# Kernel tuning notes

Measured on AMD Instinct MI355X. Metric: run time of the kernel, lower is better.

The kernel has to match this reference:

```python
import jax, jax.numpy as jnp
import numpy as np

NUM_HEADS = 12
ROPE_THETA = 100.0

def _rotate_half(x):
    x1 = x[..., ::2]
    x2 = x[..., 1::2]
    return jnp.stack((-x2, x1), axis=-1).reshape(x.shape)

def _apply_rope(x, cos, sin):
    return x * cos + _rotate_half(x) * sin

def _rope_cos_sin(h, w, head_dim, theta):
    quarter = head_dim // 4  # head_dim=64 -> 16 freq bands
    inv_freq = 1.0 / theta ** (jnp.arange(quarter, dtype=jnp.float32) / max(quarter, 1))
    y = jnp.repeat(jnp.arange(h, dtype=jnp.float32), w)   # [h*w]
    xc = jnp.tile(jnp.arange(w, dtype=jnp.float32), h)    # [h*w]
    y_freqs = y[:, None] * inv_freq[None, :]               # [N, quarter]
    x_freqs = xc[:, None] * inv_freq[None, :]
    y_ang = jnp.repeat(y_freqs, 2, axis=-1)                # [N, half]
    x_ang = jnp.repeat(x_freqs, 2, axis=-1)
    ang = jnp.concatenate([y_ang, x_ang], axis=-1)         # [N, head_dim]
    return jnp.cos(ang)[None, None], jnp.sin(ang)[None, None]  # [1,1,N,hd]

def setup_inputs() -> dict:
    key = jax.random.key(0)
    ks = jax.random.split(key, 8)
    B, S, D = 8, 1025, 768
    s = 0.02
    return {
        "x": jax.random.normal(ks[0], (B, S, D), jnp.float32),
        "q_w": jax.random.normal(ks[1], (D, D), jnp.float32) * s,
        "q_b": jax.random.normal(ks[2], (D,), jnp.float32) * s,
        "k_w": jax.random.normal(ks[3], (D, D), jnp.float32) * s,
        "v_w": jax.random.normal(ks[4], (D, D), jnp.float32) * s,
        "v_b": jax.random.normal(ks[5], (D,), jnp.float32) * s,
        "o_w": jax.random.normal(ks[6], (D, D), jnp.float32) * s,
        "o_b": jax.random.normal(ks[7], (D,), jnp.float32) * s,
        "h": 32,
        "w": 32,
        "num_prefix_tokens": 1,
    }

def reference(x, q_w, q_b, k_w, v_w, v_b, o_w, o_b, h, w, num_prefix_tokens):
    B, S, D = x.shape
    H = NUM_HEADS
    hd = D // H
    scale = hd ** -0.5
    p = num_prefix_tokens

    def proj(W, b):
        y = jnp.einsum('bsd,ed->bse', x, W)
        if b is not None:
            y = y + b
        return y.reshape(B, S, H, hd).transpose(0, 2, 1, 3)  # [B,H,S,hd]

    q = proj(q_w, q_b)
    k = proj(k_w, None)
    v = proj(v_w, v_b)

    cos, sin = _rope_cos_sin(h, w, hd, ROPE_THETA)
    q = jnp.concatenate([q[:, :, :p], _apply_rope(q[:, :, p:], cos, sin)], axis=2)
    k = jnp.concatenate([k[:, :, :p], _apply_rope(k[:, :, p:], cos, sin)], axis=2)

    attn = jnp.einsum('bhqd,bhkd->bhqk', q * scale, k)
    attn = jax.nn.softmax(attn, axis=-1)
    out = jnp.einsum('bhqk,bhkd->bhqd', attn, v)
    out = out.transpose(0, 2, 1, 3).reshape(B, S, D)
    return jnp.einsum('bsd,ed->bse', out, o_w) + o_b
```

## Files before the change

### kernel.cpp

```cpp
#include <hip/hip_runtime.h>

typedef unsigned short u16;
typedef unsigned int   u32;
typedef __attribute__((ext_vector_type(4))) short s4;
typedef __attribute__((ext_vector_type(8))) short s8;
typedef __attribute__((ext_vector_type(4))) float f4;
typedef __attribute__((ext_vector_type(16))) float f16v;

#define NB   8
#define SEQ  1025
#define DIM  768
#define NH   12
#define HD   64
#define BPAD 1040
#define MPAD 8320
#define MV   8200
#define SQP  1040
#define SKP  1088
#define NG16 68
#define NQKV 2304
#define BHT  96
#define QSCALE 0.1803368801111204f

__device__ __forceinline__ u16 f2bf(float f) {
  u32 u = __builtin_bit_cast(u32, f);
  u += 0x7fffu + ((u >> 16) & 1u);
  return (u16)(u >> 16);
}
__device__ __forceinline__ float bf2f(u16 h) {
  return __builtin_bit_cast(float, ((u32)h) << 16);
}
__device__ __forceinline__ float exp2f_(float x) {
#if __has_builtin(__builtin_amdgcn_exp2f)
  return __builtin_amdgcn_exp2f(x);
#else
  return exp2f(x);
#endif
}
__device__ __forceinline__ u32 cvtpk(float a, float b) {
  u32 r;
  asm("v_cvt_pk_bf16_f32 %0, %1, %2" : "=v"(r) : "v"(a), "v"(b));
  return r;
}

typedef const __attribute__((address_space(1))) void cas1v;
typedef __attribute__((address_space(3))) void as3v;
__device__ __forceinline__ void gload16(const void* g, void* l) {
  __builtin_amdgcn_global_load_lds((cas1v*)g, (as3v*)l, 16, 0, 0);
}

#define MFMA16(a, b, c) __builtin_amdgcn_mfma_f32_16x16x32_bf16(a, b, c, 0, 0, 0)
#define MFMA32(a, b, c) __builtin_amdgcn_mfma_f32_32x32x16_bf16(a, b, c, 0, 0, 0)

__global__ void conv_x(const float* __restrict__ x, u16* __restrict__ xb) {
  int i = blockIdx.x * 256 + threadIdx.x;
  int e = i * 4;
  int row = e / DIM, col = e - row * DIM;
  int b = row / BPAD, s = row - b * BPAD;
  s4 o;
  if (s < SEQ) {
    float4 v = *(const float4*)(x + ((size_t)(b * SEQ + s)) * DIM + col);
    o[0] = (short)f2bf(v.x); o[1] = (short)f2bf(v.y);
    o[2] = (short)f2bf(v.z); o[3] = (short)f2bf(v.w);
  } else {
    o = (s4){0, 0, 0, 0};
  }
  *(s4*)(xb + e) = o;
}

__global__ void conv_w(const float* __restrict__ qw, const float* __restrict__ kw,
                       const float* __restrict__ vw, const float* __restrict__ ow,
                       const float* __restrict__ qb, const float* __restrict__ vb,
                       u16* __restrict__ wqkv, u16* __restrict__ wo, float* __restrict__ biasq,
                       float2* __restrict__ rt) {
  int i = blockIdx.x * 256 + threadIdx.x;
  wqkv[i]           = f2bf(qw[i]);
  wqkv[i + 589824]  = f2bf(kw[i]);
  wqkv[i + 1179648] = f2bf(vw[i]);
  wo[i]             = f2bf(ow[i]);
  if (i < NQKV) biasq[i] = (i < 768) ? qb[i] : (i < 1536 ? 0.f : vb[i - 1536]);
  if (i < SEQ * 32) {
    int s = i >> 5, jj = i & 31;
    float cs = 1.f, sn = 0.f;
    if (s > 0) {
      int tok = s - 1;
      int pos = (jj < 16) ? (tok >> 5) : (tok & 31);
      int f = jj & 15;
      float ang = (float)pos * __expf((float)f * -0.28782313662425572f);
      __sincosf(ang, &sn, &cs);
    }
    rt[i] = make_float2(cs, sn);
  }
}

template <int MODE>
__global__ __launch_bounds__(256) void gemm_bt(const u16* __restrict__ A, const u16* __restrict__ Bm,
                                               float* __restrict__ Cf, const float* __restrict__ bias,
                                               u16* __restrict__ Ql, u16* __restrict__ Kl,
                                               u16* __restrict__ Vp, const float2* __restrict__ rt,
                                               int N, int K, int Mvalid, int nnt) {
  __shared__ u16 smem[16640];
  u16 (*ct)[130] = (u16(*)[130])smem;
  int tid = threadIdx.x;
  int lane = tid & 63, wave = tid >> 6;
  int g = lane >> 4, c16 = lane & 15;
  int nwg = gridDim.x, orig = blockIdx.x;
  int qd = nwg >> 3, rm = nwg & 7, xcd = orig & 7;
  int wgid = (xcd < rm ? xcd * (qd + 1) : rm * (qd + 1) + (xcd - rm) * qd) + (orig >> 3);
  int m0 = (wgid / nnt) * 128, n0 = (wgid % nnt) * 128;
  int wm = wave >> 1, wn = wave & 1;
  f4 acc[4][4] = {};

  int ldrow = wave * 16 + (lane >> 2);
  int ldk = ((lane & 3) ^ ((ldrow >> 1) & 3)) * 8;
  const u16* Asrc = A + (size_t)(m0 + ldrow) * K + ldk;
  const u16* Bsrc = Bm + (size_t)(n0 + ldrow) * K + ldk;

  auto stage = [&](int buf, int k0) {
    u16* aw = smem + buf * 4096 + wave * 512;
    u16* bw = smem + 8192 + buf * 4096 + wave * 512;
    gload16(Asrc + k0, aw);
    gload16(Asrc + 64 * K + k0, aw + 2048);
    gload16(Bsrc + k0, bw);
    gload16(Bsrc + 64 * K + k0, bw + 2048);
  };

  stage(0, 0);
  __syncthreads();
  int nk = K >> 5;
  int kx = (g ^ ((c16 >> 1) & 3)) * 8;
  for (int t = 0; t < nk; t++) {
    int buf = t & 1;
    if (t + 1 < nk) stage(buf ^ 1, (t + 1) << 5);
    s8 af[4], bf[4];
#pragma unroll
    for (int i = 0; i < 4; i++) {
      af[i] = *(const s8*)(smem + buf * 4096 + (wm * 64 + i * 16 + c16) * 32 + kx);
      bf[i] = *(const s8*)(smem + 8192 + buf * 4096 + (wn * 64 + i * 16 + c16) * 32 + kx);
    }
    __builtin_amdgcn_s_setprio(1);
#pragma unroll
    for (int i = 0; i < 4; i++)
#pragma unroll
      for (int j = 0; j < 4; j++)
        acc[i][j] = MFMA16(af[i], bf[j], acc[i][j]);
    __builtin_amdgcn_s_setprio(0);
    __syncthreads();
  }

  if (MODE == 1) {
#pragma unroll
    for (int i = 0; i < 4; i++)
#pragma unroll
      for (int j = 0; j < 4; j++) {
        int n = n0 + wn * 64 + j * 16 + c16;
        float bv = bias[n];
#pragma unroll
        for (int r = 0; r < 4; r++) {
          int m = m0 + wm * 64 + i * 16 + g * 4 + r;
          if (m < Mvalid) Cf[(size_t)m * N + n] = acc[i][j][r] + bv;
        }
      }
  } else {
    int part = (n0 >= 1536) ? 2 : (n0 >= 768 ? 1 : 0);
    float qs = (part == 0) ? QSCALE : 1.0f;
#pragma unroll
    for (int j = 0; j < 4; j++) {
      int col = wn * 64 + j * 16 + c16;
      float bv = bias[n0 + col];
      int jj = (col & 63) >> 1;
      int odd = col & 1;
#pragma unroll
      for (int i = 0; i < 4; i++) {
        int rowb = wm * 64 + i * 16 + g * 4;
#pragma unroll
        for (int r = 0; r < 4; r++) {
          float v = acc[i][j][r] + bv;
          u16 o;
          if (part < 2) {
            float vp = __shfl_xor(v, 1);
            int m = m0 + rowb + r;
            int s = m % BPAD;
            float2 t = rt[(s < SEQ ? s : SEQ - 1) * 32 + jj];
            float rv = odd ? (v * t.x + vp * t.y) : (v * t.x - vp * t.y);
            o = f2bf(rv * qs);
          } else {
            o = f2bf(v);
          }
          ct[rowb + r][col] = o;
        }
      }
    }
    __syncthreads();
    if (part < 2) {
      u16* dstB = (part == 0) ? Ql : Kl;
      int stride = (part == 0) ? SQP : SKP;
#pragma unroll
      for (int p = 0; p < 8; p++) {
        int task = p * 256 + tid;
        int row = task >> 4, cg = (task & 15) * 8;
        int m = m0 + row, b = m / BPAD, s = m - b * BPAD;
        int n = n0 + cg;
        int hq = (n >> 6) - part * NH;
        s8 v = *(const s8*)&ct[row][cg];
        *(s8*)(dstB + ((size_t)((b * NH + hq) * stride + s)) * HD + (n & 63)) = v;
      }
    } else {
#pragma unroll
      for (int p = 0; p < 4; p++) {
        int task = p * 256 + tid;
        int col = task & 127, rg = task >> 7;
        int mb = m0 + rg * 16, b = mb / BPAD, sb = mb - b * BPAD;
        int g16 = sb >> 4;
        int n = n0 + col;
        int hq = (n >> 6) - 2 * NH;
        s8 o0, o1;
#pragma unroll
        for (int k = 0; k < 16; k++) {
          int mp = (k & 3) | (((k >> 3) & 1) << 2) | (((k >> 2) & 1) << 3);
          u16 val = ct[rg * 16 + k][col];
          if (mp < 8) o0[mp] = (short)val; else o1[mp - 8] = (short)val;
        }
        u16* dst = Vp + ((size_t)((b * NH + hq) * NG16 + g16) * HD + (n & 63)) * 16;
        *(s8*)dst = o0;
        *(s8*)(dst + 8) = o1;
      }
    }
  }
}

__global__ __launch_bounds__(256) void attn_k(const u16* __restrict__ Q, const u16* __restrict__ K,
                                              const u16* __restrict__ Vp, u16* __restrict__ Ao) {
  __shared__ u16 lds[2][2][64 * 64];
  int bh = blockIdx.x;
  int tid = threadIdx.x;
  int wave = tid >> 6, lane = tid & 63;
  int q32 = lane & 31, h = lane >> 5;
  int b = bh / NH, hh = bh % NH;
  int qb = blockIdx.y * 128 + wave * 32;
  if (qb > SEQ - 32) qb = SEQ - 32;
  const u16* Qb = Q + (size_t)bh * SQP * HD;
  const u16* Kb = K + (size_t)bh * SKP * HD;
  const u16* Vb = Vp + (size_t)bh * NG16 * 1024;

  s8 qf[4];
#pragma unroll
  for (int t = 0; t < 4; t++)
    qf[t] = *(const s8*)(Qb + (size_t)(qb + q32) * HD + 16 * t + 8 * h);

  f16v o0 = {}, o1 = {};
  float mrun = -3e38f, lrun = 0.f;
  int swz = (q32 & 7) << 4;

  auto stage = [&](int buf, int c) {
#pragma unroll
    for (int i = 0; i < 2; i++) {
      int sb = i * 4096 + tid * 16;
      int row = sb >> 7;
      int ch = (sb >> 4) & 7;
      int so = (ch ^ (row & 7)) * 8;
      u16* kd = &lds[buf][0][i * 2048 + wave * 512];
      u16* vd = &lds[buf][1][i * 2048 + wave * 512];
      gload16(Kb + (size_t)(c * 64 + row) * HD + so, kd);
      gload16(Vb + c * 4096 + i * 2048 + tid * 8, vd);
    }
  };

  stage(0, 0);
  __syncthreads();

  for (int c = 0; c < 17; c++) {
    int buf = c & 1;
    if (c < 16) stage(buf ^ 1, c + 1);
    const char* Ks = (const char*)&lds[buf][0][0];
    const char* Vs = (const char*)&lds[buf][1][0];

    f16v st0 = {}, st1 = {};
    __builtin_amdgcn_s_setprio(1);
#pragma unroll
    for (int t = 0; t < 4; t++) {
      int off = (32 * t + 16 * h) ^ swz;
      s8 a0 = *(const s8*)(Ks + q32 * 128 + off);
      s8 a1 = *(const s8*)(Ks + (32 + q32) * 128 + off);
      st0 = MFMA32(a0, qf[t], st0);
      st1 = MFMA32(a1, qf[t], st1);
    }
    __builtin_amdgcn_s_setprio(0);

    s8 vf0[4], vf1[4];
#pragma unroll
    for (int s = 0; s < 4; s++) {
      vf0[s] = *(const s8*)(Vs + 2048 * s + 32 * q32 + 16 * h);
      vf1[s] = *(const s8*)(Vs + 2048 * s + 1024 + 32 * q32 + 16 * h);
    }

    if (c == 16) {
      st0[0] = h ? -3e38f : st0[0];
#pragma unroll
      for (int r = 1; r < 16; r++) st0[r] = -3e38f;
#pragma unroll
      for (int r = 0; r < 16; r++) st1[r] = -3e38f;
    }

    float mx[8];
#pragma unroll
    for (int r = 0; r < 8; r++)
      mx[r] = fmaxf(fmaxf(st0[r], st0[r + 8]), fmaxf(st1[r], st1[r + 8]));
#pragma unroll
    for (int w = 4; w >= 1; w >>= 1)
#pragma unroll
      for (int r = 0; r < w; r++) mx[r] = fmaxf(mx[r], mx[r + w]);
    float pmax = fmaxf(mx[0], __shfl_xor(mx[0], 32));

    if (!__all(pmax <= mrun + 11.5f)) {
      float mnew = fmaxf(mrun, pmax);
      float cf = exp2f_(mrun - mnew);
      lrun *= cf;
      mrun = mnew;
#pragma unroll
      for (int r = 0; r < 16; r++) {
        float c2 = __shfl(cf, (r & 3) + 8 * (r >> 2) + 4 * h);
        o0[r] *= c2;
        o1[r] *= c2;
      }
    }

    float sm[8];
#pragma unroll
    for (int r = 0; r < 16; r++) {
      st0[r] = exp2f_(st0[r] - mrun);
      st1[r] = exp2f_(st1[r] - mrun);
    }
#pragma unroll
    for (int r = 0; r < 8; r++) sm[r] = (st0[r] + st0[r + 8]) + (st1[r] + st1[r + 8]);
#pragma unroll
    for (int w = 4; w >= 1; w >>= 1)
#pragma unroll
      for (int r = 0; r < w; r++) sm[r] += sm[r + w];
    lrun += sm[0] + __shfl_xor(sm[0], 32);

    __builtin_amdgcn_s_setprio(1);
#pragma unroll
    for (int s = 0; s < 4; s++) {
      union { s8 v; u32 w[4]; } pa;
#pragma unroll
      for (int i = 0; i < 4; i++) {
        float plo = (s < 2) ? st0[8 * (s & 1) + 2 * i]     : st1[8 * (s & 1) + 2 * i];
        float phi = (s < 2) ? st0[8 * (s & 1) + 2 * i + 1] : st1[8 * (s & 1) + 2 * i + 1];
        pa.w[i] = cvtpk(plo, phi);
      }
      o0 = MFMA32(pa.v, vf0[s], o0);
      o1 = MFMA32(pa.v, vf1[s], o1);
    }
    __builtin_amdgcn_s_setprio(0);
    __syncthreads();
  }

  float rl = 1.0f / lrun;
#pragma unroll
  for (int r = 0; r < 16; r++) {
    int cr = (r & 3) + 8 * (r >> 2) + 4 * h;
    float sc = __shfl(rl, cr);
    u16* dst = Ao + (size_t)(b * SEQ + qb + cr) * DIM + hh * HD;
    dst[q32]      = f2bf(o0[r] * sc);
    dst[32 + q32] = f2bf(o1[r] * sc);
  }
}

extern "C" void kernel_launch(void* const* d_in, const int* in_sizes, int n_in,
                              void* d_out, int out_size, void* d_ws, size_t ws_size,
                              hipStream_t stream) {
  const float* x  = (const float*)d_in[0];
  const float* qw = (const float*)d_in[1];
  const float* qb = (const float*)d_in[2];
  const float* kw = (const float*)d_in[3];
  const float* vw = (const float*)d_in[4];
  const float* vb = (const float*)d_in[5];
  const float* ow = (const float*)d_in[6];
  const float* ob = (const float*)d_in[7];
  float* out = (float*)d_out;

  char* ws = (char*)d_ws;
  u16*    xb   = (u16*)(ws);
  u16*    wqkv = (u16*)(ws + 12779520);
  u16*    wo   = (u16*)(ws + 16318464);
  float*  bq   = (float*)(ws + 17498112);
  float2* rt   = (float2*)(ws + 17507328);
  u16*    Ql   = (u16*)(ws + 17769728);
  u16*    Kl   = (u16*)(ws + 30549248);
  u16*    Vp   = (u16*)(ws + 43918592);
  u16*    Ao   = xb;

  conv_x<<<6240, 256, 0, stream>>>(x, xb);
  conv_w<<<2304, 256, 0, stream>>>(qw, kw, vw, ow, qb, vb, wqkv, wo, bq, rt);
  gemm_bt<2><<<1170, 256, 0, stream>>>(xb, wqkv, nullptr, bq, Ql, Kl, Vp, rt, NQKV, DIM, MPAD, 18);
  attn_k<<<dim3(96, 9), 256, 0, stream>>>(Ql, Kl, Vp, Ao);
  gemm_bt<1><<<390, 256, 0, stream>>>(Ao, wo, out, ob, nullptr, nullptr, nullptr, rt, DIM, DIM, MV, 6);
}
```

Measured before the change: 155.6 us.

## Rewrite QKV GEMM with 256x128 tiles, 512 threads and triple-buffered K=64 pipeline

Replaces the templated QKV projection GEMM with a dedicated kernel that uses 256x128 output tiles over 8 waves, K-steps of 64, and a three-stage LDS ring fed by direct global-to-LDS loads. The loads are interleaved between two MFMA half-phases with explicit barriers and waitcnt. Sequence padding grows from 1040 to 1056 so M divides into 256-row tiles, and the workspace offsets and conversion grid are adjusted to match. The aim is more operand reuse per tile and better overlap of memory loads with MFMA work, at the cost of more padded rows, heavy LDS use (144 KB) that limits occupancy, and fragile hand-placed synchronisation.

```diff
diff --git a/kernel.cpp b/kernel.cpp
--- a/kernel.cpp
+++ b/kernel.cpp
@@ -12,10 +12,10 @@
 #define DIM  768
 #define NH   12
 #define HD   64
-#define BPAD 1040
-#define MPAD 8320
+#define BPAD 1056
+#define MPAD 8448
 #define MV   8200
-#define SQP  1040
+#define SQP  1056
 #define SKP  1088
 #define NG16 68
 #define NQKV 2304
@@ -51,6 +51,7 @@
 
 #define MFMA16(a, b, c) __builtin_amdgcn_mfma_f32_16x16x32_bf16(a, b, c, 0, 0, 0)
 #define MFMA32(a, b, c) __builtin_amdgcn_mfma_f32_32x32x16_bf16(a, b, c, 0, 0, 0)
+#define BAR() __builtin_amdgcn_s_barrier()
 
 __global__ void conv_x(const float* __restrict__ x, u16* __restrict__ xb) {
   int i = blockIdx.x * 256 + threadIdx.x;
@@ -93,14 +94,178 @@
   }
 }
 
-template <int MODE>
-__global__ __launch_bounds__(256) void gemm_bt(const u16* __restrict__ A, const u16* __restrict__ Bm,
-                                               float* __restrict__ Cf, const float* __restrict__ bias,
-                                               u16* __restrict__ Ql, u16* __restrict__ Kl,
-                                               u16* __restrict__ Vp, const float2* __restrict__ rt,
-                                               int N, int K, int Mvalid, int nnt) {
-  __shared__ u16 smem[16640];
+__global__ __launch_bounds__(512, 2) void gemm_qkv(const u16* __restrict__ A, const u16* __restrict__ Bm,
+                                                   const float* __restrict__ bias,
+                                                   u16* __restrict__ Ql, u16* __restrict__ Kl,
+                                                   u16* __restrict__ Vp, const float2* __restrict__ rt) {
+  __shared__ u16 smem[73728];
+  const int K = DIM;
+  int tid = threadIdx.x;
+  int lane = tid & 63, wave = tid >> 6;
+  int g = lane >> 4, c16 = lane & 15;
+  int wm = wave >> 1, wn = wave & 1;
+  int nwg = gridDim.x, orig = blockIdx.x;
+  int qd = nwg >> 3, rm = nwg & 7, xcd = orig & 7;
+  int wgid = (xcd < rm ? xcd * (qd + 1) : rm * (qd + 1) + (xcd - rm) * qd) + (orig >> 3);
+  int m0 = (wgid / 18) * 256, n0 = (wgid % 18) * 128;
+
+  f4 acc[4][4] = {};
+
+  int lr = lane >> 3;
+  int lc = ((lane & 7) ^ lr) * 8;
+  const u16* As0 = A  + (size_t)(m0 + wave * 8 + lr) * K + lc;
+  const u16* Bs0 = Bm + (size_t)(n0 + wave * 8 + lr) * K + lc;
+
+  auto stageA3 = [&](int sb, int ko) {
+    u16* base = smem + sb * 24576 + wave * 512;
+    gload16(As0 + ko,           base);
+    gload16(As0 + 64 * K + ko,  base + 4096);
+    gload16(As0 + 128 * K + ko, base + 8192);
+  };
+  auto stageB3 = [&](int sb, int ko) {
+    u16* baseA = smem + sb * 24576 + wave * 512;
+    u16* baseB = smem + sb * 24576 + 16384 + wave * 512;
+    gload16(As0 + 192 * K + ko, baseA + 12288);
+    gload16(Bs0 + ko,           baseB);
+    gload16(Bs0 + 64 * K + ko,  baseB + 4096);
+  };
+
+  int rsw = (c16 & 7) << 3;
+  int colk0 = (g * 8) ^ rsw;
+  int colk1 = (g * 8 + 32) ^ rsw;
+
+  stageA3(0, 0);  stageB3(0, 0);
+  stageA3(1, 64); stageB3(1, 64);
+  asm volatile("s_waitcnt vmcnt(6)" ::: "memory");
+  BAR();
+
+#pragma unroll 3
+  for (int kt = 0; kt < 12; ++kt) {
+    const u16* bp = smem + (kt % 3) * 24576;
+    int sb = (kt + 2) % 3, ko = (kt + 2) * 64;
+    bool st = kt < 10;
+    s8 bfr[4][2], afr[2][2];
+#pragma unroll
+    for (int n = 0; n < 4; n++) {
+      int rb = wn * 64 + n * 16 + c16;
+      bfr[n][0] = *(const s8*)(bp + 16384 + rb * 64 + colk0);
+      bfr[n][1] = *(const s8*)(bp + 16384 + rb * 64 + colk1);
+    }
+#pragma unroll
+    for (int m = 0; m < 2; m++) {
+      int ra = wm * 64 + m * 16 + c16;
+      afr[m][0] = *(const s8*)(bp + ra * 64 + colk0);
+      afr[m][1] = *(const s8*)(bp + ra * 64 + colk1);
+    }
+    if (st) stageA3(sb, ko);
+    BAR();
+    asm volatile("s_waitcnt lgkmcnt(0)" ::: "memory");
+    __builtin_amdgcn_s_setprio(1);
+#pragma unroll
+    for (int m = 0; m < 2; m++)
+#pragma unroll
+      for (int n = 0; n < 4; n++) {
+        acc[m][n] = MFMA16(afr[m][0], bfr[n][0], acc[m][n]);
+        acc[m][n] = MFMA16(afr[m][1], bfr[n][1], acc[m][n]);
+      }
+    __builtin_amdgcn_s_setprio(0);
+    BAR();
+    s8 af2[2][2];
+#pragma unroll
+    for (int m = 0; m < 2; m++) {
+      int ra = wm * 64 + (m + 2) * 16 + c16;
+      af2[m][0] = *(const s8*)(bp + ra * 64 + colk0);
+      af2[m][1] = *(const s8*)(bp + ra * 64 + colk1);
+    }
+    if (st) stageB3(sb, ko);
+    BAR();
+    asm volatile("s_waitcnt lgkmcnt(0)" ::: "memory");
+    __builtin_amdgcn_s_setprio(1);
+#pragma unroll
+    for (int m = 0; m < 2; m++)
+#pragma unroll
+      for (int n = 0; n < 4; n++) {
+        acc[m + 2][n] = MFMA16(af2[m][0], bfr[n][0], acc[m + 2][n]);
+        acc[m + 2][n] = MFMA16(af2[m][1], bfr[n][1], acc[m + 2][n]);
+      }
+    __builtin_amdgcn_s_setprio(0);
+    if (kt < 10)       asm volatile("s_waitcnt vmcnt(6)" ::: "memory");
+    else if (kt == 10) asm volatile("s_waitcnt vmcnt(0)" ::: "memory");
+    BAR();
+  }
+
+  __syncthreads();
   u16 (*ct)[130] = (u16(*)[130])smem;
+  int part = (n0 >= 1536) ? 2 : (n0 >= 768 ? 1 : 0);
+  float qs = (part == 0) ? QSCALE : 1.0f;
+#pragma unroll
+  for (int j = 0; j < 4; j++) {
+    int col = wn * 64 + j * 16 + c16;
+    float bv = bias[n0 + col];
+    int jj = (col & 63) >> 1;
+    int odd = col & 1;
+#pragma unroll
+    for (int i = 0; i < 4; i++) {
+      int rowb = wm * 64 + i * 16 + g * 4;
+#pragma unroll
+      for (int r = 0; r < 4; r++) {
+        float v = acc[i][j][r] + bv;
+        u16 o;
+        if (part < 2) {
+          float vp = __shfl_xor(v, 1);
+          int m = m0 + rowb + r;
+          int s = m % BPAD;
+          float2 t = rt[(s < SEQ ? s : SEQ - 1) * 32 + jj];
+          float rv = odd ? (v * t.x + vp * t.y) : (v * t.x - vp * t.y);
+          o = f2bf(rv * qs);
+        } else {
+          o = f2bf(v);
+        }
+        ct[rowb + r][col] = o;
+      }
+    }
+  }
+  __syncthreads();
+  if (part < 2) {
+    u16* dstB = (part == 0) ? Ql : Kl;
+    int stride = (part == 0) ? SQP : SKP;
+#pragma unroll
+    for (int p = 0; p < 8; p++) {
+      int task = p * 512 + tid;
+      int row = task >> 4, cg = (task & 15) * 8;
+      int m = m0 + row, b = m / BPAD, s = m - b * BPAD;
+      int n = n0 + cg;
+      int hq = (n >> 6) - part * NH;
+      s8 v = *(const s8*)&ct[row][cg];
+      *(s8*)(dstB + ((size_t)((b * NH + hq) * stride + s)) * HD + (n & 63)) = v;
+    }
+  } else {
+#pragma unroll
+    for (int p = 0; p < 4; p++) {
+      int task = p * 512 + tid;
+      int col = task & 127, rg = task >> 7;
+      int mb = m0 + rg * 16, b = mb / BPAD, sb2 = mb - b * BPAD;
+      int g16 = sb2 >> 4;
+      int n = n0 + col;
+      int hq = (n >> 6) - 2 * NH;
+      s8 o0, o1;
+#pragma unroll
+      for (int k = 0; k < 16; k++) {
+        int mp = (k & 3) | (((k >> 3) & 1) << 2) | (((k >> 2) & 1) << 3);
+        u16 val = ct[rg * 16 + k][col];
+        if (mp < 8) o0[mp] = (short)val; else o1[mp - 8] = (short)val;
+      }
+      u16* dst = Vp + ((size_t)((b * NH + hq) * NG16 + g16) * HD + (n & 63)) * 16;
+      *(s8*)dst = o0;
+      *(s8*)(dst + 8) = o1;
+    }
+  }
+}
+
+__global__ __launch_bounds__(256) void gemm_o(const u16* __restrict__ A, const u16* __restrict__ Bm,
+                                              float* __restrict__ Cf, const float* __restrict__ bias,
+                                              int N, int K, int Mvalid, int nnt) {
+  __shared__ u16 smem[16384];
   int tid = threadIdx.x;
   int lane = tid & 63, wave = tid >> 6;
   int g = lane >> 4, c16 = lane & 15;
@@ -148,85 +313,18 @@
     __syncthreads();
   }
 
-  if (MODE == 1) {
-#pragma unroll
-    for (int i = 0; i < 4; i++)
-#pragma unroll
-      for (int j = 0; j < 4; j++) {
-        int n = n0 + wn * 64 + j * 16 + c16;
-        float bv = bias[n];
-#pragma unroll
-        for (int r = 0; r < 4; r++) {
-          int m = m0 + wm * 64 + i * 16 + g * 4 + r;
-          if (m < Mvalid) Cf[(size_t)m * N + n] = acc[i][j][r] + bv;
-        }
-      }
-  } else {
-    int part = (n0 >= 1536) ? 2 : (n0 >= 768 ? 1 : 0);
-    float qs = (part == 0) ? QSCALE : 1.0f;
+#pragma unroll
+  for (int i = 0; i < 4; i++)
 #pragma unroll
     for (int j = 0; j < 4; j++) {
-      int col = wn * 64 + j * 16 + c16;
-      float bv = bias[n0 + col];
-      int jj = (col & 63) >> 1;
-      int odd = col & 1;
-#pragma unroll
-      for (int i = 0; i < 4; i++) {
-        int rowb = wm * 64 + i * 16 + g * 4;
-#pragma unroll
-        for (int r = 0; r < 4; r++) {
-          float v = acc[i][j][r] + bv;
-          u16 o;
-          if (part < 2) {
-            float vp = __shfl_xor(v, 1);
-            int m = m0 + rowb + r;
-            int s = m % BPAD;
-            float2 t = rt[(s < SEQ ? s : SEQ - 1) * 32 + jj];
-            float rv = odd ? (v * t.x + vp * t.y) : (v * t.x - vp * t.y);
-            o = f2bf(rv * qs);
-          } else {
-            o = f2bf(v);
-          }
-          ct[rowb + r][col] = o;
-        }
-      }
-    }
-    __syncthreads();
-    if (part < 2) {
-      u16* dstB = (part == 0) ? Ql : Kl;
-      int stride = (part == 0) ? SQP : SKP;
-#pragma unroll
-      for (int p = 0; p < 8; p++) {
-        int task = p * 256 + tid;
-        int row = task >> 4, cg = (task & 15) * 8;
-        int m = m0 + row, b = m / BPAD, s = m - b * BPAD;
-        int n = n0 + cg;
-        int hq = (n >> 6) - part * NH;
-        s8 v = *(const s8*)&ct[row][cg];
-        *(s8*)(dstB + ((size_t)((b * NH + hq) * stride + s)) * HD + (n & 63)) = v;
-      }
-    } else {
-#pragma unroll
-      for (int p = 0; p < 4; p++) {
-        int task = p * 256 + tid;
-        int col = task & 127, rg = task >> 7;
-        int mb = m0 + rg * 16, b = mb / BPAD, sb = mb - b * BPAD;
-        int g16 = sb >> 4;
-        int n = n0 + col;
-        int hq = (n >> 6) - 2 * NH;
-        s8 o0, o1;
-#pragma unroll
-        for (int k = 0; k < 16; k++) {
-          int mp = (k & 3) | (((k >> 3) & 1) << 2) | (((k >> 2) & 1) << 3);
-          u16 val = ct[rg * 16 + k][col];
-          if (mp < 8) o0[mp] = (short)val; else o1[mp - 8] = (short)val;
-        }
-        u16* dst = Vp + ((size_t)((b * NH + hq) * NG16 + g16) * HD + (n & 63)) * 16;
-        *(s8*)dst = o0;
-        *(s8*)(dst + 8) = o1;
-      }
-    }
-  }
+      int n = n0 + wn * 64 + j * 16 + c16;
+      float bv = bias[n];
+#pragma unroll
+      for (int r = 0; r < 4; r++) {
+        int m = m0 + wm * 64 + i * 16 + g * 4 + r;
+        if (m < Mvalid) Cf[(size_t)m * N + n] = acc[i][j][r] + bv;
+      }
+    }
 }
 
 __global__ __launch_bounds__(256) void attn_k(const u16* __restrict__ Q, const u16* __restrict__ K,
@@ -382,18 +480,18 @@
 
   char* ws = (char*)d_ws;
   u16*    xb   = (u16*)(ws);
-  u16*    wqkv = (u16*)(ws + 12779520);
-  u16*    wo   = (u16*)(ws + 16318464);
-  float*  bq   = (float*)(ws + 17498112);
-  float2* rt   = (float2*)(ws + 17507328);
-  u16*    Ql   = (u16*)(ws + 17769728);
-  u16*    Kl   = (u16*)(ws + 30549248);
-  u16*    Vp   = (u16*)(ws + 43918592);
+  u16*    wqkv = (u16*)(ws + 12976128);
+  u16*    wo   = (u16*)(ws + 16515072);
+  float*  bq   = (float*)(ws + 17694720);
+  float2* rt   = (float2*)(ws + 17703936);
+  u16*    Ql   = (u16*)(ws + 17966336);
+  u16*    Kl   = (u16*)(ws + 30942464);
+  u16*    Vp   = (u16*)(ws + 44311808);
   u16*    Ao   = xb;
 
-  conv_x<<<6240, 256, 0, stream>>>(x, xb);
+  conv_x<<<6336, 256, 0, stream>>>(x, xb);
   conv_w<<<2304, 256, 0, stream>>>(qw, kw, vw, ow, qb, vb, wqkv, wo, bq, rt);
-  gemm_bt<2><<<1170, 256, 0, stream>>>(xb, wqkv, nullptr, bq, Ql, Kl, Vp, rt, NQKV, DIM, MPAD, 18);
+  gemm_qkv<<<594, 512, 0, stream>>>(xb, wqkv, bq, Ql, Kl, Vp, rt);
   attn_k<<<dim3(96, 9), 256, 0, stream>>>(Ql, Kl, Vp, Ao);
-  gemm_bt<1><<<390, 256, 0, stream>>>(Ao, wo, out, ob, nullptr, nullptr, nullptr, rt, DIM, DIM, MV, 6);
-}
+  gemm_o<<<390, 256, 0, stream>>>(Ao, wo, out, ob, DIM, DIM, MV, 6);
+}
```

Result: slower. 161.4 us (+3.7%).

## Deepen GEMM LDS pipeline to five stages with vmcnt-based waits

Applied to the files above, without the earlier changes.

Replaces the double-buffered k-loop in the bf16 GEMM with a 5-slot ring of LDS buffers and three tiles of prefetch in flight. The loop is fully unrolled over the fixed K=768 and uses explicit vmcnt waits plus a raw barrier instead of __syncthreads. The aim is to hide global-load latency better. In exchange LDS use rises to 80KB per block, which may cut occupancy, and the manual waitcnt ordering is fragile.

```diff
diff --git a/kernel.cpp b/kernel.cpp
--- a/kernel.cpp
+++ b/kernel.cpp
@@ -51,6 +51,7 @@
 
 #define MFMA16(a, b, c) __builtin_amdgcn_mfma_f32_16x16x32_bf16(a, b, c, 0, 0, 0)
 #define MFMA32(a, b, c) __builtin_amdgcn_mfma_f32_32x32x16_bf16(a, b, c, 0, 0, 0)
+#define BAR() __builtin_amdgcn_s_barrier()
 
 __global__ void conv_x(const float* __restrict__ x, u16* __restrict__ xb) {
   int i = blockIdx.x * 256 + threadIdx.x;
@@ -98,8 +99,9 @@
                                                float* __restrict__ Cf, const float* __restrict__ bias,
                                                u16* __restrict__ Ql, u16* __restrict__ Kl,
                                                u16* __restrict__ Vp, const float2* __restrict__ rt,
-                                               int N, int K, int Mvalid, int nnt) {
-  __shared__ u16 smem[16640];
+                                               int N, int Mvalid, int nnt) {
+  __shared__ u16 smem[40960];
+  const int K = DIM;
   u16 (*ct)[130] = (u16(*)[130])smem;
   int tid = threadIdx.x;
   int lane = tid & 63, wave = tid >> 6;
@@ -117,27 +119,29 @@
   const u16* Bsrc = Bm + (size_t)(n0 + ldrow) * K + ldk;
 
   auto stage = [&](int buf, int k0) {
-    u16* aw = smem + buf * 4096 + wave * 512;
-    u16* bw = smem + 8192 + buf * 4096 + wave * 512;
+    u16* aw = smem + buf * 8192 + wave * 512;
+    u16* bw = smem + buf * 8192 + 4096 + wave * 512;
     gload16(Asrc + k0, aw);
     gload16(Asrc + 64 * K + k0, aw + 2048);
     gload16(Bsrc + k0, bw);
     gload16(Bsrc + 64 * K + k0, bw + 2048);
   };
 
-  stage(0, 0);
-  __syncthreads();
-  int nk = K >> 5;
+  stage(0, 0); stage(1, 32); stage(2, 64); stage(3, 96);
+  asm volatile("s_waitcnt vmcnt(12)" ::: "memory");
+  BAR();
+
   int kx = (g ^ ((c16 >> 1) & 3)) * 8;
-  for (int t = 0; t < nk; t++) {
-    int buf = t & 1;
-    if (t + 1 < nk) stage(buf ^ 1, (t + 1) << 5);
+#pragma unroll
+  for (int s = 0; s < 24; s++) {
+    const u16* bp = smem + (s % 5) * 8192;
     s8 af[4], bf[4];
 #pragma unroll
     for (int i = 0; i < 4; i++) {
-      af[i] = *(const s8*)(smem + buf * 4096 + (wm * 64 + i * 16 + c16) * 32 + kx);
-      bf[i] = *(const s8*)(smem + 8192 + buf * 4096 + (wn * 64 + i * 16 + c16) * 32 + kx);
-    }
+      af[i] = *(const s8*)(bp + (wm * 64 + i * 16 + c16) * 32 + kx);
+      bf[i] = *(const s8*)(bp + 4096 + (wn * 64 + i * 16 + c16) * 32 + kx);
+    }
+    if (s + 4 < 24) stage((s + 4) % 5, (s + 4) * 32);
     __builtin_amdgcn_s_setprio(1);
 #pragma unroll
     for (int i = 0; i < 4; i++)
@@ -145,7 +149,12 @@
       for (int j = 0; j < 4; j++)
         acc[i][j] = MFMA16(af[i], bf[j], acc[i][j]);
     __builtin_amdgcn_s_setprio(0);
-    __syncthreads();
+    if (s < 20)       asm volatile("s_waitcnt vmcnt(12)" ::: "memory");
+    else if (s == 20) asm volatile("s_waitcnt vmcnt(8)" ::: "memory");
+    else if (s == 21) asm volatile("s_waitcnt vmcnt(4)" ::: "memory");
+    else if (s == 22) asm volatile("s_waitcnt vmcnt(0)" ::: "memory");
+    __builtin_amdgcn_sched_barrier(0);
+    BAR();
   }
 
   if (MODE == 1) {
@@ -162,6 +171,7 @@
         }
       }
   } else {
+    __syncthreads();
     int part = (n0 >= 1536) ? 2 : (n0 >= 768 ? 1 : 0);
     float qs = (part == 0) ? QSCALE : 1.0f;
 #pragma unroll
@@ -210,8 +220,8 @@
       for (int p = 0; p < 4; p++) {
         int task = p * 256 + tid;
         int col = task & 127, rg = task >> 7;
-        int mb = m0 + rg * 16, b = mb / BPAD, sb = mb - b * BPAD;
-        int g16 = sb >> 4;
+        int mb = m0 + rg * 16, b = mb / BPAD, sb2 = mb - b * BPAD;
+        int g16 = sb2 >> 4;
         int n = n0 + col;
         int hq = (n >> 6) - 2 * NH;
         s8 o0, o1;
@@ -393,7 +403,7 @@
 
   conv_x<<<6240, 256, 0, stream>>>(x, xb);
   conv_w<<<2304, 256, 0, stream>>>(qw, kw, vw, ow, qb, vb, wqkv, wo, bq, rt);
-  gemm_bt<2><<<1170, 256, 0, stream>>>(xb, wqkv, nullptr, bq, Ql, Kl, Vp, rt, NQKV, DIM, MPAD, 18);
+  gemm_bt<2><<<1170, 256, 0, stream>>>(xb, wqkv, nullptr, bq, Ql, Kl, Vp, rt, NQKV, MPAD, 18);
   attn_k<<<dim3(96, 9), 256, 0, stream>>>(Ql, Kl, Vp, Ao);
-  gemm_bt<1><<<390, 256, 0, stream>>>(Ao, wo, out, ob, nullptr, nullptr, nullptr, rt, DIM, DIM, MV, 6);
-}
+  gemm_bt<1><<<390, 256, 0, stream>>>(Ao, wo, out, ob, nullptr, nullptr, nullptr, rt, DIM, MV, 6);
+}
```

Result: no change. 157.9 us (+1.5%).
